# Kernel tuning notes

Measured on AMD Instinct MI355X. Metric: run time of the kernel, lower is better.

The kernel has to match this reference:

```python
import jax, jax.numpy as jnp
import numpy as np

B, OBS, T, H = 4096, 16, 32, 512  # batch, encoder length, decode seq_len, hidden_size


def _lstm_cell(x, h, c, Wi, Wh, b):
    # PyTorch gate order: i, f, g, o. b = b_ih + b_hh (mathematically identical).
    g = x @ Wi.T + h @ Wh.T + b
    i, f, gg, o = jnp.split(g, 4, axis=-1)
    c = jax.nn.sigmoid(f) * c + jax.nn.sigmoid(i) * jnp.tanh(gg)
    h = jax.nn.sigmoid(o) * jnp.tanh(c)
    return h, c


def _encode(xs, Wi, Wh, b):
    # xs: [B, T, 4]; returns final (h, c), zero initial state as in nn.LSTM.
    def step(carry, x):
        h, c = _lstm_cell(x, carry[0], carry[1], Wi, Wh, b)
        return (h, c), None
    z = jnp.zeros((xs.shape[0], H), xs.dtype)
    (h, c), _ = jax.lax.scan(step, (z, z), jnp.swapaxes(xs, 0, 1))
    return h, c


def setup_inputs() -> dict:
    key = jax.random.key(0)
    ks = jax.random.split(key, 22)
    s = 0.05
    p = lambda k, shape: (jax.random.normal(k, shape, jnp.float32) * s)
    return {
        "speed": jax.random.normal(ks[0], (B, OBS, 4), jnp.float32),
        "pos": jax.random.normal(ks[1], (B, OBS, 4), jnp.float32),
        "enc_s_Wi": p(ks[2], (4 * H, 4)), "enc_s_Wh": p(ks[3], (4 * H, H)), "enc_s_b": p(ks[4], (4 * H,)),
        "enc_p_Wi": p(ks[5], (4 * H, 4)), "enc_p_Wh": p(ks[6], (4 * H, H)), "enc_p_b": p(ks[7], (4 * H,)),
        "dec_s_Wi": p(ks[8], (4 * H, 4)), "dec_s_Wh": p(ks[9], (4 * H, H)), "dec_s_b": p(ks[10], (4 * H,)),
        "dec_i_Wi": p(ks[11], (4 * H, 4)), "dec_i_Wh": p(ks[12], (4 * H, H)), "dec_i_b": p(ks[13], (4 * H,)),
        "W_fs": p(ks[14], (4, H)), "b_fs": p(ks[15], (4,)),
        "W_fc": p(ks[16], (2, H)), "b_fc": p(ks[17], (2,)),
        "W_emb": p(ks[18], (4, 2)), "b_emb": p(ks[19], (4,)),
    }


def reference(speed, pos,
              enc_s_Wi, enc_s_Wh, enc_s_b,
              enc_p_Wi, enc_p_Wh, enc_p_b,
              dec_s_Wi, dec_s_Wh, dec_s_b,
              dec_i_Wi, dec_i_Wh, dec_i_b,
              W_fs, b_fs, W_fc, b_fc, W_emb, b_emb):
    h_se, c_se = _encode(speed, enc_s_Wi, enc_s_Wh, enc_s_b)
    h_pe, c_pe = _encode(pos, enc_p_Wi, enc_p_Wh, enc_p_b)
    h_s, c_s = h_se + h_pe, c_se + c_pe
    h_i, c_i = h_s, c_s
    last_speed = speed[:, -1, :]
    last_pos = pos[:, -1, :]

    def step(carry, _):
        h_s, c_s, h_i, c_i, ls, lp = carry
        h_s, c_s = _lstm_cell(ls, h_s, c_s, dec_s_Wi, dec_s_Wh, dec_s_b)
        h_i, c_i = _lstm_cell(lp, h_i, c_i, dec_i_Wi, dec_i_Wh, dec_i_b)
        sp = jnp.clip(h_s @ W_fs.T + b_fs, -100.0, 100.0)        # Hardtanh(-100, 100)
        it = jax.nn.relu(h_i @ W_fc.T + b_fc)                     # fc_crossing
        ls = jax.lax.stop_gradient(sp)                            # .detach()
        lp = jax.lax.stop_gradient(jax.nn.relu(it @ W_emb.T + b_emb))  # pos_embedding(.).detach()
        return (h_s, c_s, h_i, c_i, ls, lp), (sp, jax.nn.softmax(it, axis=1))

    carry0 = (h_s, c_s, h_i, c_i, last_speed, last_pos)
    _, (speed_seq, cross_seq) = jax.lax.scan(step, carry0, None, length=T)
    speed_outputs = jnp.swapaxes(speed_seq, 0, 1)   # [B, T, 4]
    # Faithful to the source bug: intention_outputs is never accumulated, so the
    # returned crossing_outputs holds ONLY the last step's softmax: [B, 1, 2].
    crossing_outputs = cross_seq[-1][:, None, :]
    return speed_outputs, crossing_outputs
```

## Files before the change

### kernel.cpp

```cpp
#include <hip/hip_runtime.h>
#include <stdint.h>

#define H 512
#define KAUG 544
#define KT_N 34
#define NT_N 64
#define LROW 552
#define NROW 32
#define WMAT_ELEMS (NT_N * KT_N * 512)
#define T_DEC 32
#define B_TOT 4096

typedef __attribute__((ext_vector_type(8))) short short8;
typedef __attribute__((ext_vector_type(16))) float floatx16;

__device__ __forceinline__ unsigned short f2bf(float x) {
  union { float f; unsigned int u; } v; v.f = x;
  unsigned int u = v.u;
  return (unsigned short)((u + 0x7FFFu + ((u >> 16) & 1u)) >> 16);
}
__device__ __forceinline__ float bf2f(unsigned short s) {
  union { unsigned int u; float f; } v; v.u = ((unsigned int)s) << 16;
  return v.f;
}
__device__ __forceinline__ float sigm(float x) { return 1.0f / (1.0f + __expf(-x)); }
__device__ __forceinline__ float tanh_f(float x) {
  return 2.0f / (1.0f + __expf(-2.0f * x)) - 1.0f;
}

__global__ void prep_weights(
    const float* __restrict__ Wh_s, const float* __restrict__ Wi_s, const float* __restrict__ b_s,
    const float* __restrict__ Wh_p, const float* __restrict__ Wi_p, const float* __restrict__ b_p,
    const float* __restrict__ Wh_d, const float* __restrict__ Wi_d, const float* __restrict__ b_d,
    const float* __restrict__ Wh_i, const float* __restrict__ Wi_i, const float* __restrict__ b_i,
    short* __restrict__ wpack)
{
  int idx = blockIdx.x * 256 + threadIdx.x;
  const int per = 2048 * KAUG;
  if (idx >= 4 * per) return;
  int mat = idx / per;
  int rem = idx - mat * per;
  int n = rem / KAUG;
  int ka = rem - n * KAUG;
  const float* Wh; const float* Wi; const float* bb;
  if (mat == 0)      { Wh = Wh_s; Wi = Wi_s; bb = b_s; }
  else if (mat == 1) { Wh = Wh_p; Wi = Wi_p; bb = b_p; }
  else if (mat == 2) { Wh = Wh_d; Wi = Wi_d; bb = b_d; }
  else               { Wh = Wh_i; Wi = Wi_i; bb = b_i; }
  float v;
  if (ka < 512)      v = Wh[n * 512 + ka];
  else if (ka < 516) v = Wi[n * 4 + (ka - 512)];
  else if (ka == 516) v = bb[n];
  else               v = 0.0f;
  int nt = n >> 5, ni = n & 31;
  int kt = ka >> 4, kh = (ka >> 3) & 1, ks = ka & 7;
  int lanep = kh * 32 + ni;
  wpack[(size_t)mat * WMAT_ELEMS + ((((size_t)nt * KT_N + kt) * 64 + lanep) << 3) + ks] =
      (short)f2bf(v);
}

__device__ __forceinline__ void lstm_step_mfma(
    const short* hl, const short* __restrict__ wm,
    int lane, int wv, float c_reg[2][16], float hnew[2][16])
{
  int arow = lane & 31, ahalf = lane >> 5;
  const short* aptr = hl + arow * LROW + ahalf * 8;
  #pragma unroll
  for (int jt = 0; jt < 2; ++jt) {
    int ntbase = wv * 2 + jt;
    const short* bp0 = wm + (((size_t)(0 * 16 + ntbase) * KT_N) << 9) + (lane << 3);
    const short* bp1 = wm + (((size_t)(1 * 16 + ntbase) * KT_N) << 9) + (lane << 3);
    const short* bp2 = wm + (((size_t)(2 * 16 + ntbase) * KT_N) << 9) + (lane << 3);
    const short* bp3 = wm + (((size_t)(3 * 16 + ntbase) * KT_N) << 9) + (lane << 3);
    floatx16 ai = (floatx16)0.0f, af = (floatx16)0.0f, ag = (floatx16)0.0f, ao = (floatx16)0.0f;
    #pragma unroll 2
    for (int kt = 0; kt < KT_N; ++kt) {
      short8 a  = *(const short8*)(aptr + kt * 16);
      short8 b0 = *(const short8*)(bp0 + (kt << 9));
      short8 b1 = *(const short8*)(bp1 + (kt << 9));
      short8 b2 = *(const short8*)(bp2 + (kt << 9));
      short8 b3 = *(const short8*)(bp3 + (kt << 9));
      ai = __builtin_amdgcn_mfma_f32_32x32x16_bf16(a, b0, ai, 0, 0, 0);
      af = __builtin_amdgcn_mfma_f32_32x32x16_bf16(a, b1, af, 0, 0, 0);
      ag = __builtin_amdgcn_mfma_f32_32x32x16_bf16(a, b2, ag, 0, 0, 0);
      ao = __builtin_amdgcn_mfma_f32_32x32x16_bf16(a, b3, ao, 0, 0, 0);
    }
    #pragma unroll
    for (int r = 0; r < 16; ++r) {
      float si = sigm(ai[r]);
      float sf = sigm(af[r]);
      float tg = tanh_f(ag[r]);
      float so = sigm(ao[r]);
      float cn = sf * c_reg[jt][r] + si * tg;
      c_reg[jt][r] = cn;
      hnew[jt][r] = so * tanh_f(cn);
    }
  }
}

__device__ __forceinline__ void write_h(short* hl, int lane, int wv, const float hnew[2][16]) {
  int arow = lane & 31, ahalf = lane >> 5;
  #pragma unroll
  for (int jt = 0; jt < 2; ++jt) {
    int col = wv * 64 + jt * 32 + arow;
    #pragma unroll
    for (int r = 0; r < 16; ++r) {
      int row = (r & 3) + ((r >> 2) << 3) + (ahalf << 2);
      hl[row * LROW + col] = (short)f2bf(hnew[jt][r]);
    }
  }
}

__global__ __launch_bounds__(512) void lstm_encoder(
    const float* __restrict__ speed, const float* __restrict__ pos,
    const short* __restrict__ wpack,
    short* __restrict__ h_enc, float* __restrict__ c_enc)
{
  __shared__ short hl[NROW * LROW];
  int tid = threadIdx.x;
  int b = blockIdx.x;
  int xcd = b & 7, slot = b >> 3;
  int enc = xcd >> 2;
  int rg = slot * 4 + (xcd & 3);
  int r0 = rg * 32;
  const float* xin = enc ? pos : speed;
  const short* wm = wpack + (size_t)enc * WMAT_ELEMS;

  for (int i = tid; i < NROW * LROW; i += 512) hl[i] = 0;
  __syncthreads();
  if (tid < 32) hl[tid * LROW + 516] = (short)0x3F80;
  if (tid < 128) {
    int r = tid >> 2, c = tid & 3;
    hl[r * LROW + 512 + c] = (short)f2bf(xin[(r0 + r) * 64 + c]);
  }
  __syncthreads();

  int lane = tid & 63, wv = tid >> 6;
  float c_reg[2][16];
  #pragma unroll
  for (int jt = 0; jt < 2; ++jt)
    #pragma unroll
    for (int r = 0; r < 16; ++r) c_reg[jt][r] = 0.0f;
  float hnew[2][16];

  for (int t = 0; t < 16; ++t) {
    lstm_step_mfma(hl, wm, lane, wv, c_reg, hnew);
    __syncthreads();
    write_h(hl, lane, wv, hnew);
    if (t < 15 && tid < 128) {
      int r = tid >> 2, c = tid & 3;
      hl[r * LROW + 512 + c] = (short)f2bf(xin[(r0 + r) * 64 + (t + 1) * 4 + c]);
    }
    __syncthreads();
  }

  for (int i = tid; i < 32 * 512; i += 512) {
    int r = i >> 9, k = i & 511;
    h_enc[((size_t)(enc * B_TOT + r0 + r) << 9) + k] = hl[r * LROW + k];
  }
  int arow = lane & 31, ahalf = lane >> 5;
  #pragma unroll
  for (int jt = 0; jt < 2; ++jt) {
    int col = wv * 64 + jt * 32 + arow;
    #pragma unroll
    for (int r = 0; r < 16; ++r) {
      int row = (r & 3) + ((r >> 2) << 3) + (ahalf << 2);
      c_enc[((size_t)(enc * B_TOT + r0 + row) << 9) + col] = c_reg[jt][r];
    }
  }
}

__global__ __launch_bounds__(512) void lstm_decoder(
    const float* __restrict__ speed, const float* __restrict__ pos,
    const short* __restrict__ wpack,
    const short* __restrict__ h_enc, const float* __restrict__ c_enc,
    const float* __restrict__ W_fs, const float* __restrict__ b_fs,
    const float* __restrict__ W_fc, const float* __restrict__ b_fc,
    const float* __restrict__ W_emb, const float* __restrict__ b_emb,
    float* __restrict__ out)
{
  __shared__ short hl[NROW * LROW];
  int tid = threadIdx.x;
  int b = blockIdx.x;
  int xcd = b & 7, slot = b >> 3;
  int chain = xcd >> 2;
  int rg = slot * 4 + (xcd & 3);
  int r0 = rg * 32;
  const short* wm = wpack + (size_t)(2 + chain) * WMAT_ELEMS;

  for (int i = tid; i < NROW * LROW; i += 512) hl[i] = 0;
  __syncthreads();
  for (int i = tid; i < 32 * 512; i += 512) {
    int r = i >> 9, k = i & 511;
    float h0 = bf2f((unsigned short)h_enc[((size_t)(r0 + r) << 9) + k])
             + bf2f((unsigned short)h_enc[((size_t)(B_TOT + r0 + r) << 9) + k]);
    hl[r * LROW + k] = (short)f2bf(h0);
  }
  if (tid < 32) hl[tid * LROW + 516] = (short)0x3F80;
  {
    const float* last = chain ? pos : speed;
    if (tid < 128) {
      int r = tid >> 2, c = tid & 3;
      hl[r * LROW + 512 + c] = (short)f2bf(last[(r0 + r) * 64 + 60 + c]);
    }
  }
  int lane = tid & 63, wv = tid >> 6;
  int arow = lane & 31, ahalf = lane >> 5;
  float c_reg[2][16];
  #pragma unroll
  for (int jt = 0; jt < 2; ++jt) {
    int col = wv * 64 + jt * 32 + arow;
    #pragma unroll
    for (int r = 0; r < 16; ++r) {
      int row = (r & 3) + ((r >> 2) << 3) + (ahalf << 2);
      size_t gi = ((size_t)(r0 + row) << 9) + col;
      c_reg[jt][r] = c_enc[gi] + c_enc[gi + (((size_t)B_TOT) << 9)];
    }
  }
  __syncthreads();

  float wro[4][8];
  float hb[4];
  float we[8], be[4];
  if (chain == 0) {
    #pragma unroll
    for (int o = 0; o < 4; ++o) {
      #pragma unroll
      for (int j = 0; j < 8; ++j) wro[o][j] = W_fs[o * 512 + lane * 8 + j];
      hb[o] = b_fs[o];
    }
  } else {
    #pragma unroll
    for (int o = 0; o < 2; ++o) {
      #pragma unroll
      for (int j = 0; j < 8; ++j) wro[o][j] = W_fc[o * 512 + lane * 8 + j];
      hb[o] = b_fc[o];
    }
    #pragma unroll
    for (int j = 0; j < 8; ++j) we[j] = W_emb[j];
    #pragma unroll
    for (int o = 0; o < 4; ++o) be[o] = b_emb[o];
  }

  float hnew[2][16];
  for (int t = 0; t < T_DEC; ++t) {
    lstm_step_mfma(hl, wm, lane, wv, c_reg, hnew);
    __syncthreads();
    write_h(hl, lane, wv, hnew);
    __syncthreads();
    #pragma unroll 1
    for (int r = 0; r < 4; ++r) {
      int row = wv * 4 + r;
      const short8 hvs = *(const short8*)(hl + row * LROW + lane * 8);
      float hv[8];
      #pragma unroll
      for (int j = 0; j < 8; ++j) hv[j] = bf2f((unsigned short)hvs[j]);
      if (chain == 0) {
        float p0 = 0.f, p1 = 0.f, p2 = 0.f, p3 = 0.f;
        #pragma unroll
        for (int j = 0; j < 8; ++j) {
          p0 += hv[j] * wro[0][j];
          p1 += hv[j] * wro[1][j];
          p2 += hv[j] * wro[2][j];
          p3 += hv[j] * wro[3][j];
        }
        #pragma unroll
        for (int off = 32; off > 0; off >>= 1) {
          p0 += __shfl_xor(p0, off);
          p1 += __shfl_xor(p1, off);
          p2 += __shfl_xor(p2, off);
          p3 += __shfl_xor(p3, off);
        }
        float s0 = fminf(fmaxf(p0 + hb[0], -100.0f), 100.0f);
        float s1 = fminf(fmaxf(p1 + hb[1], -100.0f), 100.0f);
        float s2 = fminf(fmaxf(p2 + hb[2], -100.0f), 100.0f);
        float s3 = fminf(fmaxf(p3 + hb[3], -100.0f), 100.0f);
        if (lane < 4) {
          float v = (lane == 0) ? s0 : (lane == 1) ? s1 : (lane == 2) ? s2 : s3;
          out[(size_t)(r0 + row) * 128 + t * 4 + lane] = v;
          hl[row * LROW + 512 + lane] = (short)f2bf(v);
        }
      } else {
        float p0 = 0.f, p1 = 0.f;
        #pragma unroll
        for (int j = 0; j < 8; ++j) {
          p0 += hv[j] * wro[0][j];
          p1 += hv[j] * wro[1][j];
        }
        #pragma unroll
        for (int off = 32; off > 0; off >>= 1) {
          p0 += __shfl_xor(p0, off);
          p1 += __shfl_xor(p1, off);
        }
        float it0 = fmaxf(p0 + hb[0], 0.0f);
        float it1 = fmaxf(p1 + hb[1], 0.0f);
        if (lane < 4) {
          float lp = fmaxf(we[lane * 2] * it0 + we[lane * 2 + 1] * it1 + be[lane], 0.0f);
          hl[row * LROW + 512 + lane] = (short)f2bf(lp);
        }
        if (t == T_DEC - 1 && lane < 2) {
          float m = fmaxf(it0, it1);
          float e0 = __expf(it0 - m), e1 = __expf(it1 - m);
          float v = ((lane == 0) ? e0 : e1) / (e0 + e1);
          out[(size_t)524288 + (size_t)(r0 + row) * 2 + lane] = v;
        }
      }
    }
    __syncthreads();
  }
}

extern "C" void kernel_launch(void* const* d_in, const int* in_sizes, int n_in,
                              void* d_out, int out_size, void* d_ws, size_t ws_size,
                              hipStream_t stream)
{
  const float* speed    = (const float*)d_in[0];
  const float* pos      = (const float*)d_in[1];
  const float* enc_s_Wi = (const float*)d_in[2];
  const float* enc_s_Wh = (const float*)d_in[3];
  const float* enc_s_b  = (const float*)d_in[4];
  const float* enc_p_Wi = (const float*)d_in[5];
  const float* enc_p_Wh = (const float*)d_in[6];
  const float* enc_p_b  = (const float*)d_in[7];
  const float* dec_s_Wi = (const float*)d_in[8];
  const float* dec_s_Wh = (const float*)d_in[9];
  const float* dec_s_b  = (const float*)d_in[10];
  const float* dec_i_Wi = (const float*)d_in[11];
  const float* dec_i_Wh = (const float*)d_in[12];
  const float* dec_i_b  = (const float*)d_in[13];
  const float* W_fs     = (const float*)d_in[14];
  const float* b_fs     = (const float*)d_in[15];
  const float* W_fc     = (const float*)d_in[16];
  const float* b_fc     = (const float*)d_in[17];
  const float* W_emb    = (const float*)d_in[18];
  const float* b_emb    = (const float*)d_in[19];
  float* out = (float*)d_out;

  char* ws = (char*)d_ws;
  short* wpack = (short*)ws;
  short* h_enc = (short*)(ws + 8912896);
  float* c_enc = (float*)(ws + 17301504);

  prep_weights<<<17408, 256, 0, stream>>>(
      enc_s_Wh, enc_s_Wi, enc_s_b,
      enc_p_Wh, enc_p_Wi, enc_p_b,
      dec_s_Wh, dec_s_Wi, dec_s_b,
      dec_i_Wh, dec_i_Wi, dec_i_b,
      wpack);
  lstm_encoder<<<256, 512, 0, stream>>>(speed, pos, wpack, h_enc, c_enc);
  lstm_decoder<<<256, 512, 0, stream>>>(speed, pos, wpack, h_enc, c_enc,
                                        W_fs, b_fs, W_fc, b_fc, W_emb, b_emb, out);
}
```

Measured before the change: 1.534 ms.

## Interleave gate weight tiles, trim K padding, and use fast reciprocal activations

Repacks the bf16 weight matrix so the four gate tiles for each k-step sit next to each other, which lets one pointer walk them with sequential loads. The padded K dimension shrinks from 544 to 528 because bias plus inputs fit in one extra 16-wide tile, removing one MFMA k-step per gate. Sigmoid, tanh and the softmax divide now use the hardware approximate reciprocal instead of a true division, which slightly lowers precision. The unroll factor is raised to 3 to match the 33-step loop.

Result: faster. 1.315 ms (-14.3%).

```diff
diff --git a/kernel.cpp b/kernel.cpp
--- a/kernel.cpp
+++ b/kernel.cpp
@@ -2,12 +2,11 @@
 #include <stdint.h>
 
 #define H 512
-#define KAUG 544
-#define KT_N 34
-#define NT_N 64
-#define LROW 552
+#define KAUG 528
+#define KT_N 33
+#define LROW 536
 #define NROW 32
-#define WMAT_ELEMS (NT_N * KT_N * 512)
+#define WMAT_ELEMS (16 * KT_N * 4 * 512)
 #define T_DEC 32
 #define B_TOT 4096
 
@@ -23,9 +22,10 @@
   union { unsigned int u; float f; } v; v.u = ((unsigned int)s) << 16;
   return v.f;
 }
-__device__ __forceinline__ float sigm(float x) { return 1.0f / (1.0f + __expf(-x)); }
+__device__ __forceinline__ float rcpf(float x) { return __builtin_amdgcn_rcpf(x); }
+__device__ __forceinline__ float sigm(float x) { return rcpf(1.0f + __expf(-x)); }
 __device__ __forceinline__ float tanh_f(float x) {
-  return 2.0f / (1.0f + __expf(-2.0f * x)) - 1.0f;
+  return 1.0f - 2.0f * rcpf(1.0f + __expf(2.0f * x));
 }
 
 __global__ void prep_weights(
@@ -52,11 +52,11 @@
   else if (ka < 516) v = Wi[n * 4 + (ka - 512)];
   else if (ka == 516) v = bb[n];
   else               v = 0.0f;
-  int nt = n >> 5, ni = n & 31;
+  int g = n >> 9, ntL = (n >> 5) & 15, ni = n & 31;
   int kt = ka >> 4, kh = (ka >> 3) & 1, ks = ka & 7;
   int lanep = kh * 32 + ni;
-  wpack[(size_t)mat * WMAT_ELEMS + ((((size_t)nt * KT_N + kt) * 64 + lanep) << 3) + ks] =
-      (short)f2bf(v);
+  wpack[(size_t)mat * WMAT_ELEMS +
+        (((((size_t)ntL * KT_N + kt) * 4 + g) << 9) + (lanep << 3) + ks)] = (short)f2bf(v);
 }
 
 __device__ __forceinline__ void lstm_step_mfma(
@@ -67,19 +67,17 @@
   const short* aptr = hl + arow * LROW + ahalf * 8;
   #pragma unroll
   for (int jt = 0; jt < 2; ++jt) {
-    int ntbase = wv * 2 + jt;
-    const short* bp0 = wm + (((size_t)(0 * 16 + ntbase) * KT_N) << 9) + (lane << 3);
-    const short* bp1 = wm + (((size_t)(1 * 16 + ntbase) * KT_N) << 9) + (lane << 3);
-    const short* bp2 = wm + (((size_t)(2 * 16 + ntbase) * KT_N) << 9) + (lane << 3);
-    const short* bp3 = wm + (((size_t)(3 * 16 + ntbase) * KT_N) << 9) + (lane << 3);
+    int ntL = wv * 2 + jt;
+    const short* bp = wm + (size_t)ntL * (KT_N * 4 * 512) + (lane << 3);
     floatx16 ai = (floatx16)0.0f, af = (floatx16)0.0f, ag = (floatx16)0.0f, ao = (floatx16)0.0f;
-    #pragma unroll 2
+    #pragma unroll 3
     for (int kt = 0; kt < KT_N; ++kt) {
       short8 a  = *(const short8*)(aptr + kt * 16);
-      short8 b0 = *(const short8*)(bp0 + (kt << 9));
-      short8 b1 = *(const short8*)(bp1 + (kt << 9));
-      short8 b2 = *(const short8*)(bp2 + (kt << 9));
-      short8 b3 = *(const short8*)(bp3 + (kt << 9));
+      short8 b0 = *(const short8*)(bp);
+      short8 b1 = *(const short8*)(bp + 512);
+      short8 b2 = *(const short8*)(bp + 1024);
+      short8 b3 = *(const short8*)(bp + 1536);
+      bp += 2048;
       ai = __builtin_amdgcn_mfma_f32_32x32x16_bf16(a, b0, ai, 0, 0, 0);
       af = __builtin_amdgcn_mfma_f32_32x32x16_bf16(a, b1, af, 0, 0, 0);
       ag = __builtin_amdgcn_mfma_f32_32x32x16_bf16(a, b2, ag, 0, 0, 0);
@@ -301,7 +299,7 @@
         if (t == T_DEC - 1 && lane < 2) {
           float m = fmaxf(it0, it1);
           float e0 = __expf(it0 - m), e1 = __expf(it1 - m);
-          float v = ((lane == 0) ? e0 : e1) / (e0 + e1);
+          float v = ((lane == 0) ? e0 : e1) * rcpf(e0 + e1);
           out[(size_t)524288 + (size_t)(r0 + row) * 2 + lane] = v;
         }
       }
@@ -338,10 +336,10 @@
 
   char* ws = (char*)d_ws;
   short* wpack = (short*)ws;
-  short* h_enc = (short*)(ws + 8912896);
-  float* c_enc = (float*)(ws + 17301504);
-
-  prep_weights<<<17408, 256, 0, stream>>>(
+  short* h_enc = (short*)(ws + 8650752);
+  float* c_enc = (float*)(ws + 17039360);
+
+  prep_weights<<<16896, 256, 0, stream>>>(
       enc_s_Wh, enc_s_Wi, enc_s_b,
       enc_p_Wh, enc_p_Wi, enc_p_b,
       dec_s_Wh, dec_s_Wi, dec_s_b,
```
